# Kernel optimization log

Hardware: AMD Instinct MI355X
Metric: run time of the kernel (lower is better)

Reference implementation:

```python
import jax, jax.numpy as jnp
import numpy as np

K_SIZE = 5
SIGMA_IMG = 0.2
SIGMA_VGG = 0.02
BN_EPS = 1e-5
NORM = 2.0  # 2 * len(GPU_IDS), assuming 1 device


def _window_shifts(x, k):
    # x: (n, C, H, W) -> (n, C, H, W, k*k) neighbor values for every offset in
    # the k x k window, zero-padded at image borders.
    r = k // 2
    n, C, H, W = x.shape
    xp = jnp.pad(x, ((0, 0), (0, 0), (r, r), (r, r)))
    cols = [xp[:, :, di:di + H, dj:dj + W] for di in range(k) for dj in range(k)]
    return jnp.stack(cols, axis=-1)


def _modularity(img, seg, k, sigma):
    # img: (n, C, H, W) feature map; seg: (n, K, H, W) soft assignments.
    n, K, H, W = seg.shape
    seg2 = _window_shifts(seg, k)                                  # (n,K,H,W,kk)
    img2 = _window_shifts(img, k)                                  # (n,C,H,W,kk)
    valid = _window_shifts(jnp.ones((1, 1, H, W), img.dtype), k)[:, 0]  # (1,H,W,kk)
    d2 = ((img[..., None] - img2) ** 2).sum(axis=1)                # (n,H,W,kk)
    w12 = jax.lax.stop_gradient(jnp.exp(-d2 / (2.0 * sigma * sigma)) * valid)
    # numerator: sum over pixels & pairs of p1*p2*w12, per (n, K)
    num = jnp.einsum('nkhw,nkhwp,nhwp->nk', seg, seg2, w12)
    # p1 (sum over pairs of p1/n_pairs) == seg; w1 = sum over pairs of w12
    w1 = w12.sum(axis=-1)                                          # (n,H,W)
    den = jnp.einsum('nhw,nkhw->nk', w1, seg)
    rel = num / den                                                # (n,K)
    return rel.sum(axis=1) / (K * n)                               # (n,)


def _conv(x, w, b):
    y = jax.lax.conv_general_dilated(x, w, (1, 1), 'SAME',
                                     dimension_numbers=('NCHW', 'OIHW', 'NCHW'))
    return y + b[None, :, None, None]


def _maxpool2(x):
    return jax.lax.reduce_window(x, -jnp.inf, jax.lax.max,
                                 (1, 1, 2, 2), (1, 1, 2, 2), 'VALID')


def _avgpool2(x):
    n, c, h, w = x.shape
    return x.reshape(n, c, h // 2, 2, w // 2, 2).mean(axis=(3, 5))


def _vgg8(x, w1, b1, w2, b2, w3, b3, w4, b4):
    # VGG16 features[:8]: conv1_1, conv1_2, maxpool, conv2_1, conv2_2 (relu each)
    x = jax.nn.relu(_conv(x, w1, b1))
    x = jax.nn.relu(_conv(x, w2, b2))
    x = _maxpool2(x)
    x = jax.nn.relu(_conv(x, w3, b3))
    x = jax.nn.relu(_conv(x, w4, b4))
    return x


def _batchnorm(x):
    # fresh BatchNorm2d in training mode (weight=1, bias=0), then detach
    m = x.mean(axis=(0, 2, 3), keepdims=True)
    v = x.var(axis=(0, 2, 3), keepdims=True)
    return jax.lax.stop_gradient((x - m) / jnp.sqrt(v + BN_EPS))


def setup_inputs() -> dict:
    key = jax.random.key(0)
    ks = jax.random.split(key, 6)
    images = jax.random.uniform(ks[0], (4, 3, 128, 128), jnp.float32)
    seg = jax.random.uniform(ks[1], (4, 8, 128, 128), jnp.float32)
    segmentation = seg / seg.sum(axis=1, keepdims=True)
    w1 = jax.random.normal(ks[2], (64, 3, 3, 3), jnp.float32) * 0.1
    w2 = jax.random.normal(ks[3], (64, 64, 3, 3), jnp.float32) * 0.05
    w3 = jax.random.normal(ks[4], (128, 64, 3, 3), jnp.float32) * 0.05
    w4 = jax.random.normal(ks[5], (128, 128, 3, 3), jnp.float32) * 0.03
    return {'images': images, 'segmentation': segmentation,
            'w1': w1, 'b1': jnp.zeros(64), 'w2': w2, 'b2': jnp.zeros(64),
            'w3': w3, 'b3': jnp.zeros(128), 'w4': w4, 'b4': jnp.zeros(128)}


def reference(images, segmentation, w1, b1, w2, b2, w3, b3, w4, b4):
    fich = _batchnorm(_vgg8(images, w1, b1, w2, b2, w3, b3, w4, b4))  # (n,128,64,64)
    images_n = _batchnorm(images)
    down_seg = segmentation
    while down_seg.shape[-1] != fich.shape[-1]:
        down_seg = _avgpool2(down_seg)
    loss = (_modularity(fich, down_seg, K_SIZE, SIGMA_VGG).sum()
            + _modularity(images_n, segmentation, K_SIZE, SIGMA_IMG).sum())
    return loss / NORM
```

## Files before the change

### kernel.cpp

```cpp
#include <hip/hip_runtime.h>
#include <hip/hip_bf16.h>
#include <math.h>

typedef __attribute__((ext_vector_type(8))) short short8;
typedef __attribute__((ext_vector_type(4))) float floatx4;
typedef unsigned short ushortT;

__device__ inline short f2bf(float v) {
    __hip_bfloat16 h = __float2bfloat16(v);
    union { __hip_bfloat16 h; short s; } u; u.h = h; return u.s;
}

#define OFF_C2    0
#define OFF_PAD4  8388608
#define OFF_FICH  12849152
#define OFF_PAD2  21237760
#define OFF_PAD3  29890560
#define OFF_WP2   32120832
#define OFF_WP3   32194560
#define OFF_WP4   32342016
#define OFF_ST    33947648
#define OFF_P64   33951744
#define OFF_P128  33968128
#define OFF_PBN   34033664
#define OFF_PIMG  34295808

__global__ __launch_bounds__(256) void prologue(
    char* ws, const float* __restrict__ images,
    const float* __restrict__ w2, const float* __restrict__ w3,
    const float* __restrict__ w4)
{
    int b = blockIdx.x;
    int tid = threadIdx.x;

    if (b < 162) {
        int t = b * 256 + tid;
        short* base; int Hp, Wp, C; int idx;
        if (t < 16512)      { base = (short*)(ws + OFF_PAD2); Hp = 130; Wp = 130; C = 64;  idx = t; }
        else if (t < 24832) { base = (short*)(ws + OFF_PAD3); Hp = 66;  Wp = 66;  C = 64;  idx = t - 16512; }
        else if (t < 41472) { base = (short*)(ws + OFF_PAD4); Hp = 66;  Wp = 66;  C = 128; idx = t - 24832; }
        else return;
        int c8 = idx % (C / 8); int rest = idx / (C / 8);
        int haloPx = 2 * Wp + 2 * (Hp - 2);
        int p = rest % haloPx; int n = rest / haloPx;
        int y, x;
        if (p < Wp)          { y = 0;      x = p; }
        else if (p < 2 * Wp) { y = Hp - 1; x = p - Wp; }
        else { int j = p - 2 * Wp; y = 1 + (j >> 1); x = (j & 1) ? (Wp - 1) : 0; }
        short8 z = {0, 0, 0, 0, 0, 0, 0, 0};
        *(short8*)&base[((size_t)((n * Hp + y) * Wp) + x) * C + c8 * 8] = z;
        return;
    }
    if (b < 1170) {
        int e = (b - 162) * 256 + tid;
        const float* w; short* wp; int CIN, NTALL;
        if (e < 36864)       { w = w2; wp = (short*)(ws + OFF_WP2); CIN = 64;  NTALL = 4; }
        else if (e < 110592) { e -= 36864;  w = w3; wp = (short*)(ws + OFF_WP3); CIN = 64;  NTALL = 8; }
        else if (e < 258048) { e -= 110592; w = w4; wp = (short*)(ws + OFF_WP4); CIN = 128; NTALL = 8; }
        else return;
        int j = e & 7; int L = (e >> 3) & 63; int rest = e >> 9;
        int nt = rest % NTALL; int rest2 = rest / NTALL;
        int KT = CIN / 32;
        int kt = rest2 % KT; int t = rest2 / KT;
        int oc = nt * 16 + (L & 15);
        int ci = kt * 32 + (L >> 4) * 8 + j;
        wp[e] = f2bf(w[((size_t)oc * CIN + ci) * 9 + t]);
        return;
    }
    {
        float* part = (float*)(ws + OFF_PIMG);
        int bb = b - 1170;
        int c = bb >> 6, chunk = bb & 63;
        int base = chunk * 1024 + tid;
        float s = 0.f, s2 = 0.f;
#pragma unroll
        for (int k = 0; k < 4; ++k) {
            int i = base + k * 256;
            int n = i >> 14, hw = i & 16383;
            float v = images[(((size_t)(n * 3 + c)) << 14) + hw];
            s += v; s2 = fmaf(v, v, s2);
        }
        __shared__ float rs[256], rs2[256];
        rs[tid] = s; rs2[tid] = s2;
        __syncthreads();
        for (int k = 128; k > 0; k >>= 1) {
            if (tid < k) { rs[tid] += rs[tid + k]; rs2[tid] += rs2[tid + k]; }
            __syncthreads();
        }
        if (tid == 0) { part[bb * 2] = rs[0]; part[bb * 2 + 1] = rs2[0]; }
    }
}

__global__ __launch_bounds__(256) void conv1_bf16(
    const float* __restrict__ in, const float* __restrict__ w,
    const float* __restrict__ b, short* __restrict__ outp)
{
    int bid = blockIdx.x;
    int txt = bid & 7; bid >>= 3;
    int tyt = bid & 7; bid >>= 3;
    int ocg = bid & 7; bid >>= 3;
    int n = bid;
    int x0 = txt * 16, y0 = tyt * 16;
    int tid = threadIdx.x;
    int tx = tid & 15, ty = tid >> 4;

    __shared__ float lds[3 * 720];
    for (int i = tid; i < 972; i += 256) {
        int cc = i / 324; int rem = i - cc * 324;
        int r = rem / 18, c = rem - r * 18;
        int y = y0 - 1 + r, x = x0 - 1 + c;
        float v = 0.f;
        if ((unsigned)y < 128u && (unsigned)x < 128u)
            v = in[((size_t)(n * 3 + cc) * 128 + y) * 128 + x];
        lds[cc * 720 + r * 40 + c] = v;
    }
    __syncthreads();

    float acc[8];
#pragma unroll
    for (int oc = 0; oc < 8; ++oc) acc[oc] = 0.f;
    const float* w_g = w + (size_t)(ocg * 8) * 27;
#pragma unroll
    for (int cc = 0; cc < 3; ++cc) {
        const float* base = &lds[cc * 720 + ty * 40 + tx];
        float i00 = base[0],  i01 = base[1],  i02 = base[2];
        float i10 = base[40], i11 = base[41], i12 = base[42];
        float i20 = base[80], i21 = base[81], i22 = base[82];
        const float* wp = w_g + cc * 9;
#pragma unroll
        for (int oc = 0; oc < 8; ++oc) {
            const float* wq = wp + oc * 27;
            float a = acc[oc];
            a = fmaf(wq[0], i00, a); a = fmaf(wq[1], i01, a); a = fmaf(wq[2], i02, a);
            a = fmaf(wq[3], i10, a); a = fmaf(wq[4], i11, a); a = fmaf(wq[5], i12, a);
            a = fmaf(wq[6], i20, a); a = fmaf(wq[7], i21, a); a = fmaf(wq[8], i22, a);
            acc[oc] = a;
        }
    }
    int oy = y0 + ty, ox = x0 + tx;
    short* o = outp + ((size_t)(n * 130 + oy + 1) * 130 + ox + 1) * 64 + ocg * 8;
#pragma unroll
    for (int oc = 0; oc < 8; ++oc) {
        float v = fmaxf(acc[oc] + b[ocg * 8 + oc], 0.f);
        o[oc] = f2bf(v);
    }
}

template<int CIN, int COUT, int H, int W, int OUTMODE>
__global__ __launch_bounds__(256) void conv_mfma2(
    const short* __restrict__ inp, const short* __restrict__ wp,
    const float* __restrict__ bias, void* __restrict__ outv)
{
    constexpr int KT = CIN / 32;
    constexpr int NTALL = COUT / 16;
    constexpr int NTB = COUT / 64;
    constexpr int TPR = W / 64;
    constexpr int Hp = H + 2, Wp = W + 2;

    int bm = blockIdx.x / NTB;
    int bn = blockIdx.x - bm * NTB;
    int n = bm / (H * TPR);
    int rem = bm - n * (H * TPR);
    int y = rem / TPR;
    int x0 = (rem - y * TPR) * 64;

    int tid = threadIdx.x;
    int wv = tid >> 6, lane = tid & 63;
    int lm = lane & 15, q = lane >> 4;
    int px0 = x0 + 16 * wv;
    int ntb = bn * 4;

    floatx4 acc[4];
#pragma unroll
    for (int t = 0; t < 4; ++t) acc[t] = (floatx4){0.f, 0.f, 0.f, 0.f};

    const short* a_m = inp + lm * CIN + q * 8;
    const short* wbase = wp + ((size_t)ntb * 64 + lane) * 8;

    for (int kt = 0; kt < KT; ++kt) {
        int kofs = kt * 32;
#pragma unroll
        for (int r = 0; r < 3; ++r) {
            const short* arow = a_m + (size_t)((n * Hp + y + r) * Wp + px0) * CIN + kofs;
#pragma unroll
            for (int s = 0; s < 3; ++s) {
                short8 av = *(const short8*)(arow + s * CIN);
                const short* bp = wbase + (size_t)(((r * 3 + s) * KT + kt) * NTALL) * 512;
                short8 b0 = *(const short8*)bp;
                short8 b1 = *(const short8*)(bp + 512);
                short8 b2 = *(const short8*)(bp + 1024);
                short8 b3 = *(const short8*)(bp + 1536);
                acc[0] = __builtin_amdgcn_mfma_f32_16x16x32_bf16(av, b0, acc[0], 0, 0, 0);
                acc[1] = __builtin_amdgcn_mfma_f32_16x16x32_bf16(av, b1, acc[1], 0, 0, 0);
                acc[2] = __builtin_amdgcn_mfma_f32_16x16x32_bf16(av, b2, acc[2], 0, 0, 0);
                acc[3] = __builtin_amdgcn_mfma_f32_16x16x32_bf16(av, b3, acc[3], 0, 0, 0);
            }
        }
    }

#pragma unroll
    for (int t = 0; t < 4; ++t) {
        int oc = (ntb + t) * 16 + lm;
        float bs = bias[oc];
#pragma unroll
        for (int i = 0; i < 4; ++i) {
            int px = px0 + q * 4 + i;
            float v = fmaxf(acc[t][i] + bs, 0.f);
            if constexpr (OUTMODE == 0) {
                ((short*)outv)[((size_t)(n * H + y) * W + px) * COUT + oc] = f2bf(v);
            } else if constexpr (OUTMODE == 1) {
                ((short*)outv)[((size_t)(n * Hp + y + 1) * Wp + px + 1) * COUT + oc] = f2bf(v);
            } else {
                ((float*)outv)[((size_t)(n * H + y) * W + px) * COUT + oc] = v;
            }
        }
    }
}

__global__ __launch_bounds__(256) void maxpool_nhwc(const ushortT* __restrict__ in,
                                                    ushortT* __restrict__ outp)
{
    int gid = blockIdx.x * 256 + threadIdx.x;
    int c8 = gid & 7; int rest = gid >> 3;
    int xo = rest & 63, yo = (rest >> 6) & 63, n = rest >> 12;
    const ushortT* p = in + ((size_t)(n * 128 + yo * 2) * 128 + xo * 2) * 64 + c8 * 8;
    const ushortT* p01 = p + 64;
    const ushortT* p10 = p + 128 * 64;
    const ushortT* p11 = p10 + 64;
    ushortT* o = outp + ((size_t)(n * 66 + yo + 1) * 66 + xo + 1) * 64 + c8 * 8;
#pragma unroll
    for (int j = 0; j < 8; ++j) {
        ushortT a = p[j] > p01[j] ? p[j] : p01[j];
        ushortT b = p10[j] > p11[j] ? p10[j] : p11[j];
        o[j] = a > b ? a : b;
    }
}

__global__ __launch_bounds__(256) void bnsum_nhwc(const float* __restrict__ x,
                                                  float* __restrict__ part)
{
    int tid = threadIdx.x;
    int c = tid & 127;
    int h = tid >> 7;
    int p0 = blockIdx.x * 64 + h * 32;
    float s = 0.f, s2 = 0.f;
    for (int p = p0; p < p0 + 32; ++p) {
        float v = x[(size_t)p * 128 + c];
        s += v; s2 = fmaf(v, v, s2);
    }
    __shared__ float rs[256], rs2[256];
    rs[tid] = s; rs2[tid] = s2;
    __syncthreads();
    if (tid < 128) {
        part[(size_t)blockIdx.x * 256 + tid] = rs[tid] + rs[tid + 128];
        part[(size_t)blockIdx.x * 256 + 128 + tid] = rs2[tid] + rs2[tid + 128];
    }
}

__global__ __launch_bounds__(256) void stats_fin(const float* __restrict__ part,
                                                 float* __restrict__ st)
{
    int c = blockIdx.x;
    int t = threadIdx.x;
    float s  = part[(size_t)t * 256 + c];
    float s2 = part[(size_t)t * 256 + 128 + c];
    __shared__ float rs[256], rs2[256];
    rs[t] = s; rs2[t] = s2;
    __syncthreads();
    for (int k = 128; k > 0; k >>= 1) {
        if (t < k) { rs[t] += rs[t + k]; rs2[t] += rs2[t + k]; }
        __syncthreads();
    }
    if (t == 0) {
        float mean = rs[0] * (1.f / 16384.f);
        float var = rs2[0] * (1.f / 16384.f) - mean * mean;
        st[c] = 1.f / sqrtf(var + 1e-5f);
    }
}

__global__ __launch_bounds__(256) void modularity64_v5(
    const float* __restrict__ xt,
    const float* __restrict__ seg,
    const float* __restrict__ st,
    float* __restrict__ part)
{
    __shared__ float fl[4 * 2880];
    __shared__ float sl[8][12][14];

    int tid = threadIdx.x;
    int w = tid >> 6, lane = tid & 63;
    int tx = lane & 7, ty = lane >> 3;
    int obid = blockIdx.x;
    int bid = obid;
    int bx = bid & 7; bid >>= 3;
    int by = bid & 7; bid >>= 3;
    int n = bid;
    int x0 = bx * 8, y0 = by * 8;

    for (int i = tid; i < 8 * 144; i += 256) {
        int k = i / 144;
        int rem = i - k * 144;
        int r = rem / 12, c = rem - r * 12;
        int y = y0 - 2 + r, x = x0 - 2 + c;
        float v = 0.f;
        if ((unsigned)y < 64u && (unsigned)x < 64u) {
            const float* p = seg + ((size_t)(n * 8 + k) * 128 + 2 * y) * 128 + 2 * x;
            float2 a = *(const float2*)p;
            float2 b = *(const float2*)(p + 128);
            v = 0.25f * ((a.x + a.y) + (b.x + b.y));
        }
        sl[k][r][c] = v;
    }

    float* slab = fl + w * 2880;

    float d2p[25];
#pragma unroll
    for (int di = 0; di < 5; ++di)
#pragma unroll
        for (int dj = 0; dj < 5; ++dj) {
            int y2 = y0 + ty + di - 2, x2 = x0 + tx + dj - 2;
            float bias = ((unsigned)y2 < 64u && (unsigned)x2 < 64u) ? 0.f : 1e30f;
            d2p[di * 5 + dj] = (w == 0) ? bias : 0.f;
        }

    for (int r8 = 0; r8 < 2; ++r8) {
        int ch0 = w * 32 + r8 * 16;
        for (int i = lane; i < 576; i += 64) {
            int pix = i >> 2, q = i & 3;
            int r = pix / 12, c = pix - r * 12;
            int y = y0 - 2 + r, x = x0 - 2 + c;
            float4 v = make_float4(0.f, 0.f, 0.f, 0.f);
            if ((unsigned)y < 64u && (unsigned)x < 64u) {
                v = *(const float4*)&xt[((size_t)((n * 64 + y) * 64 + x)) * 128 + ch0 + q * 4];
                float4 sv = *(const float4*)&st[ch0 + q * 4];
                v.x *= sv.x; v.y *= sv.y; v.z *= sv.z; v.w *= sv.w;
            }
            *(float4*)&slab[(r * 12 + c) * 20 + q * 4] = v;
        }

        const float* ctr = &slab[((ty + 2) * 12 + tx + 2) * 20];
        float4 c0 = *(const float4*)(ctr + 0);
        float4 c1 = *(const float4*)(ctr + 4);
        float4 c2 = *(const float4*)(ctr + 8);
        float4 c3 = *(const float4*)(ctr + 12);
#pragma unroll
        for (int di = 0; di < 5; ++di)
#pragma unroll
            for (int dj = 0; dj < 5; ++dj) {
                const float* np = &slab[((ty + di) * 12 + tx + dj) * 20];
                float4 v0 = *(const float4*)(np + 0);
                float4 v1 = *(const float4*)(np + 4);
                float4 v2 = *(const float4*)(np + 8);
                float4 v3 = *(const float4*)(np + 12);
                float d = d2p[di * 5 + dj];
                float e;
                e = c0.x - v0.x; d = fmaf(e, e, d);
                e = c0.y - v0.y; d = fmaf(e, e, d);
                e = c0.z - v0.z; d = fmaf(e, e, d);
                e = c0.w - v0.w; d = fmaf(e, e, d);
                e = c1.x - v1.x; d = fmaf(e, e, d);
                e = c1.y - v1.y; d = fmaf(e, e, d);
                e = c1.z - v1.z; d = fmaf(e, e, d);
                e = c1.w - v1.w; d = fmaf(e, e, d);
                e = c2.x - v2.x; d = fmaf(e, e, d);
                e = c2.y - v2.y; d = fmaf(e, e, d);
                e = c2.z - v2.z; d = fmaf(e, e, d);
                e = c2.w - v2.w; d = fmaf(e, e, d);
                e = c3.x - v3.x; d = fmaf(e, e, d);
                e = c3.y - v3.y; d = fmaf(e, e, d);
                e = c3.z - v3.z; d = fmaf(e, e, d);
                e = c3.w - v3.w; d = fmaf(e, e, d);
                d2p[di * 5 + dj] = d;
            }
    }

#pragma unroll
    for (int j = 0; j < 25; ++j) slab[lane * 25 + j] = d2p[j];
    __syncthreads();

    const float minus_inv2s2 = -1.0f / (2.0f * 0.02f * 0.02f);
    for (int i = tid; i < 1600; i += 256) {
        float d = fl[i] + fl[2880 + i] + fl[5760 + i] + fl[8640 + i];
        fl[i] = expf(d * minus_inv2s2);
    }
    __syncthreads();

    float wgt[25];
    float w1 = 0.f;
#pragma unroll
    for (int j = 0; j < 25; ++j) { wgt[j] = fl[lane * 25 + j]; w1 += wgt[j]; }
#pragma unroll
    for (int kk = 0; kk < 2; ++kk) {
        int k = w * 2 + kk;
        float s = 0.f;
#pragma unroll
        for (int di = 0; di < 5; ++di)
#pragma unroll
            for (int dj = 0; dj < 5; ++dj)
                s = fmaf(wgt[di * 5 + dj], sl[k][ty + di][tx + dj], s);
        float sc = sl[k][ty + 2][tx + 2];
        float numk = s * sc;
        float denk = w1 * sc;
#pragma unroll
        for (int sh = 32; sh > 0; sh >>= 1) {
            numk += __shfl_xor(numk, sh, 64);
            denk += __shfl_xor(denk, sh, 64);
        }
        if (lane == 0) {
            part[(size_t)obid * 16 + k * 2] = numk;
            part[(size_t)obid * 16 + k * 2 + 1] = denk;
        }
    }
}

__global__ __launch_bounds__(256) void modularity128_v6(
    const float* __restrict__ img,
    const float* __restrict__ pimg,
    const float* __restrict__ seg,
    float* __restrict__ part)
{
    __shared__ float il[12][12][4];
    __shared__ float sl[8][12][14];
    __shared__ float stm[6];

    int t = threadIdx.x;
    int w = t >> 6, lane = t & 63;
    int tx = lane & 7, ty = lane >> 3;

    if (t < 64) {
#pragma unroll
        for (int ch = 0; ch < 3; ++ch) {
            float s  = pimg[(ch * 64 + t) * 2];
            float s2 = pimg[(ch * 64 + t) * 2 + 1];
#pragma unroll
            for (int sh = 32; sh > 0; sh >>= 1) {
                s += __shfl_xor(s, sh, 64);
                s2 += __shfl_xor(s2, sh, 64);
            }
            if (t == 0) {
                float mean = s * (1.f / 65536.f);
                float var = s2 * (1.f / 65536.f) - mean * mean;
                stm[ch] = mean;
                stm[3 + ch] = 1.f / sqrtf(var + 1e-5f);
            }
        }
    }

    int obid = blockIdx.x;
    int bid = obid;
    int bx = bid & 15; bid >>= 4;
    int by = bid & 15; bid >>= 4;
    int n = bid;
    int x0 = bx * 8, y0 = by * 8;

    for (int i = t; i < 8 * 144; i += 256) {
        int k = i / 144;
        int rem = i - k * 144;
        int r = rem / 12, c = rem - r * 12;
        int y = y0 - 2 + r, x = x0 - 2 + c;
        float v = 0.f;
        if ((unsigned)y < 128u && (unsigned)x < 128u)
            v = seg[((size_t)(n * 8 + k) * 128 + y) * 128 + x];
        sl[k][r][c] = v;
    }
    __syncthreads();

    float mn0 = stm[0], mn1 = stm[1], mn2 = stm[2];
    float rs0 = stm[3], rs1 = stm[4], rs2 = stm[5];

    for (int i = t; i < 432; i += 256) {
        int ch = i / 144; int pix = i - ch * 144;
        int r = pix / 12, c = pix - r * 12;
        int y = y0 - 2 + r, x = x0 - 2 + c;
        float v = 0.f;
        if ((unsigned)y < 128u && (unsigned)x < 128u) {
            float raw = img[(((size_t)(n * 3 + ch)) << 14) + y * 128 + x];
            float mn = ch == 0 ? mn0 : (ch == 1 ? mn1 : mn2);
            float rs = ch == 0 ? rs0 : (ch == 1 ? rs1 : rs2);
            v = (raw - mn) * rs;
        }
        il[r][c][ch] = v;
    }
    __syncthreads();

    const float minus_inv2s2 = -1.0f / (2.0f * 0.2f * 0.2f);
    float c0 = il[ty + 2][tx + 2][0];
    float c1 = il[ty + 2][tx + 2][1];
    float c2 = il[ty + 2][tx + 2][2];

    float wgt[25];
    float w1 = 0.f;
#pragma unroll
    for (int di = 0; di < 5; ++di)
#pragma unroll
        for (int dj = 0; dj < 5; ++dj) {
            int y2 = y0 + ty + di - 2, x2 = x0 + tx + dj - 2;
            float bias = ((unsigned)y2 < 128u && (unsigned)x2 < 128u) ? 0.f : 1e30f;
            const float* np = &il[ty + di][tx + dj][0];
            float e0 = c0 - np[0], e1 = c1 - np[1], e2 = c2 - np[2];
            float d = bias + fmaf(e2, e2, fmaf(e1, e1, e0 * e0));
            float wv = expf(d * minus_inv2s2);
            wgt[di * 5 + dj] = wv;
            w1 += wv;
        }

#pragma unroll
    for (int kk = 0; kk < 2; ++kk) {
        int k = w * 2 + kk;
        float s = 0.f;
#pragma unroll
        for (int di = 0; di < 5; ++di)
#pragma unroll
            for (int dj = 0; dj < 5; ++dj)
                s = fmaf(wgt[di * 5 + dj], sl[k][ty + di][tx + dj], s);
        float sc = sl[k][ty + 2][tx + 2];
        float numk = s * sc;
        float denk = w1 * sc;
#pragma unroll
        for (int sft = 32; sft > 0; sft >>= 1) {
            numk += __shfl_xor(numk, sft, 64);
            denk += __shfl_xor(denk, sft, 64);
        }
        if (lane == 0) {
            part[(size_t)obid * 16 + k * 2] = numk;
            part[(size_t)obid * 16 + k * 2 + 1] = denk;
        }
    }
}

__global__ __launch_bounds__(1024) void reduce_finalize(
    const float* __restrict__ p64, const float* __restrict__ p128,
    float* __restrict__ out)
{
    int t = threadIdx.x;
    int j = t >> 4, s = t & 15;
    float num = 0.f, den = 0.f;
    if (j < 32) {
        int n = j >> 3, k = j & 7;
#pragma unroll
        for (int i = 0; i < 4; ++i) {
            int b = s * 4 + i;
            const float* p = p64 + ((size_t)(n * 64 + b)) * 16 + k * 2;
            num += p[0]; den += p[1];
        }
    } else {
        int jj = j - 32; int n = jj >> 3, k = jj & 7;
#pragma unroll
        for (int i = 0; i < 16; ++i) {
            int b = s * 16 + i;
            const float* p = p128 + ((size_t)(n * 256 + b)) * 16 + k * 2;
            num += p[0]; den += p[1];
        }
    }
#pragma unroll
    for (int sh = 8; sh > 0; sh >>= 1) {
        num += __shfl_xor(num, sh, 16);
        den += __shfl_xor(den, sh, 16);
    }
    __shared__ float rn[64], rd[64];
    if (s == 0) { rn[j] = num; rd[j] = den; }
    __syncthreads();
    if (t < 64) {
        float v = rn[t] / rd[t];
#pragma unroll
        for (int sh = 32; sh > 0; sh >>= 1) v += __shfl_xor(v, sh, 64);
        if (t == 0) out[0] = v * (1.0f / 64.0f);
    }
}

extern "C" void kernel_launch(void* const* d_in, const int* in_sizes, int n_in,
                              void* d_out, int out_size, void* d_ws, size_t ws_size,
                              hipStream_t stream)
{
    const float* images = (const float*)d_in[0];
    const float* seg    = (const float*)d_in[1];
    const float* w1 = (const float*)d_in[2]; const float* b1 = (const float*)d_in[3];
    const float* w2 = (const float*)d_in[4]; const float* b2 = (const float*)d_in[5];
    const float* w3 = (const float*)d_in[6]; const float* b3 = (const float*)d_in[7];
    const float* w4 = (const float*)d_in[8]; const float* b4 = (const float*)d_in[9];
    float* out = (float*)d_out;
    char* ws = (char*)d_ws;
    short* C2   = (short*)(ws + OFF_C2);
    short* PAD2 = (short*)(ws + OFF_PAD2);
    short* PAD3 = (short*)(ws + OFF_PAD3);
    short* PAD4 = (short*)(ws + OFF_PAD4);
    float* FICH = (float*)(ws + OFF_FICH);
    short* WP2  = (short*)(ws + OFF_WP2);
    short* WP3  = (short*)(ws + OFF_WP3);
    short* WP4  = (short*)(ws + OFF_WP4);
    float* ST   = (float*)(ws + OFF_ST);
    float* P64  = (float*)(ws + OFF_P64);
    float* P128 = (float*)(ws + OFF_P128);
    float* PBN  = (float*)(ws + OFF_PBN);
    float* PIMG = (float*)(ws + OFF_PIMG);

    prologue<<<1362, 256, 0, stream>>>(ws, images, w2, w3, w4);

    conv1_bf16<<<2048, 256, 0, stream>>>(images, w1, b1, PAD2);
    conv_mfma2<64, 64, 128, 128, 0><<<1024, 256, 0, stream>>>(PAD2, WP2, b2, C2);
    maxpool_nhwc<<<512, 256, 0, stream>>>((const ushortT*)C2, (ushortT*)PAD3);
    conv_mfma2<64, 128, 64, 64, 1><<<512, 256, 0, stream>>>(PAD3, WP3, b3, PAD4);
    conv_mfma2<128, 128, 64, 64, 2><<<512, 256, 0, stream>>>(PAD4, WP4, b4, FICH);

    bnsum_nhwc<<<256, 256, 0, stream>>>(FICH, PBN);
    stats_fin<<<128, 256, 0, stream>>>(PBN, ST);

    modularity64_v5<<<256, 256, 0, stream>>>(FICH, seg, ST, P64);
    modularity128_v6<<<1024, 256, 0, stream>>>(images, PIMG, seg, P128);
    reduce_finalize<<<1, 1024, 0, stream>>>(P64, P128, out);
}
```

Baseline: 185.5 us.

## Fuse conv1 into prologue, maxpool into conv2, BN stats into conv4, merge modularity

Conv1 now runs as extra blocks of the prologue kernel. Conv2 is rewritten to compute two output rows per block and apply the 2x2 maxpool in registers, writing straight into the padded conv3 input, so the full-resolution intermediate buffer disappears. Conv4 accumulates per-channel sum and sum-of-squares for batchnorm in its epilogue, removing the separate pass that re-read the feature map. The two modularity kernels are merged into one interleaved launch. Together these cut launch count and global memory round trips, at the cost of more complex kernels, a new partial-sum layout for the stats, and some loss of tiling flexibility in conv2.

Result: faster. 166.7 us (-10.1%).

```diff
diff --git a/kernel.cpp b/kernel.cpp
--- a/kernel.cpp
+++ b/kernel.cpp
@@ -27,11 +27,67 @@
 
 __global__ __launch_bounds__(256) void prologue(
     char* ws, const float* __restrict__ images,
+    const float* __restrict__ w1, const float* __restrict__ b1,
     const float* __restrict__ w2, const float* __restrict__ w3,
     const float* __restrict__ w4)
 {
+    __shared__ float plds[3 * 720];
+    __shared__ float rs[256], rs2[256];
+
     int b = blockIdx.x;
     int tid = threadIdx.x;
+
+    if (b >= 1362) {
+        int bid = b - 1362;
+        int txt = bid & 7; bid >>= 3;
+        int tyt = bid & 7; bid >>= 3;
+        int ocg = bid & 7; bid >>= 3;
+        int n = bid;
+        int x0 = txt * 16, y0 = tyt * 16;
+        int tx = tid & 15, ty = tid >> 4;
+        short* outp = (short*)(ws + OFF_PAD2);
+
+        for (int i = tid; i < 972; i += 256) {
+            int cc = i / 324; int rem = i - cc * 324;
+            int r = rem / 18, c = rem - r * 18;
+            int y = y0 - 1 + r, x = x0 - 1 + c;
+            float v = 0.f;
+            if ((unsigned)y < 128u && (unsigned)x < 128u)
+                v = images[((size_t)(n * 3 + cc) * 128 + y) * 128 + x];
+            plds[cc * 720 + r * 40 + c] = v;
+        }
+        __syncthreads();
+
+        float acc[8];
+#pragma unroll
+        for (int oc = 0; oc < 8; ++oc) acc[oc] = 0.f;
+        const float* w_g = w1 + (size_t)(ocg * 8) * 27;
+#pragma unroll
+        for (int cc = 0; cc < 3; ++cc) {
+            const float* base = &plds[cc * 720 + ty * 40 + tx];
+            float i00 = base[0],  i01 = base[1],  i02 = base[2];
+            float i10 = base[40], i11 = base[41], i12 = base[42];
+            float i20 = base[80], i21 = base[81], i22 = base[82];
+            const float* wp = w_g + cc * 9;
+#pragma unroll
+            for (int oc = 0; oc < 8; ++oc) {
+                const float* wq = wp + oc * 27;
+                float a = acc[oc];
+                a = fmaf(wq[0], i00, a); a = fmaf(wq[1], i01, a); a = fmaf(wq[2], i02, a);
+                a = fmaf(wq[3], i10, a); a = fmaf(wq[4], i11, a); a = fmaf(wq[5], i12, a);
+                a = fmaf(wq[6], i20, a); a = fmaf(wq[7], i21, a); a = fmaf(wq[8], i22, a);
+                acc[oc] = a;
+            }
+        }
+        int oy = y0 + ty, ox = x0 + tx;
+        short* o = outp + ((size_t)(n * 130 + oy + 1) * 130 + ox + 1) * 64 + ocg * 8;
+#pragma unroll
+        for (int oc = 0; oc < 8; ++oc) {
+            float v = fmaxf(acc[oc] + b1[ocg * 8 + oc], 0.f);
+            o[oc] = f2bf(v);
+        }
+        return;
+    }
 
     if (b < 162) {
         int t = b * 256 + tid;
@@ -80,7 +136,6 @@
             float v = images[(((size_t)(n * 3 + c)) << 14) + hw];
             s += v; s2 = fmaf(v, v, s2);
         }
-        __shared__ float rs[256], rs2[256];
         rs[tid] = s; rs2[tid] = s2;
         __syncthreads();
         for (int k = 128; k > 0; k >>= 1) {
@@ -91,58 +146,85 @@
     }
 }
 
-__global__ __launch_bounds__(256) void conv1_bf16(
-    const float* __restrict__ in, const float* __restrict__ w,
-    const float* __restrict__ b, short* __restrict__ outp)
-{
+__global__ __launch_bounds__(256) void conv2_pool(
+    const short* __restrict__ inp,
+    const short* __restrict__ wp,
+    const float* __restrict__ bias,
+    short* __restrict__ outp)
+{
+    constexpr int CIN = 64;
+    constexpr int Hp = 130, Wp = 130;
+
     int bid = blockIdx.x;
-    int txt = bid & 7; bid >>= 3;
-    int tyt = bid & 7; bid >>= 3;
-    int ocg = bid & 7; bid >>= 3;
+    int xtb = bid & 1; bid >>= 1;
+    int yp = bid & 63; bid >>= 6;
     int n = bid;
-    int x0 = txt * 16, y0 = tyt * 16;
+    int y0 = yp * 2;
+    int x0 = xtb * 64;
+
     int tid = threadIdx.x;
-    int tx = tid & 15, ty = tid >> 4;
-
-    __shared__ float lds[3 * 720];
-    for (int i = tid; i < 972; i += 256) {
-        int cc = i / 324; int rem = i - cc * 324;
-        int r = rem / 18, c = rem - r * 18;
-        int y = y0 - 1 + r, x = x0 - 1 + c;
-        float v = 0.f;
-        if ((unsigned)y < 128u && (unsigned)x < 128u)
-            v = in[((size_t)(n * 3 + cc) * 128 + y) * 128 + x];
-        lds[cc * 720 + r * 40 + c] = v;
-    }
-    __syncthreads();
-
-    float acc[8];
-#pragma unroll
-    for (int oc = 0; oc < 8; ++oc) acc[oc] = 0.f;
-    const float* w_g = w + (size_t)(ocg * 8) * 27;
-#pragma unroll
-    for (int cc = 0; cc < 3; ++cc) {
-        const float* base = &lds[cc * 720 + ty * 40 + tx];
-        float i00 = base[0],  i01 = base[1],  i02 = base[2];
-        float i10 = base[40], i11 = base[41], i12 = base[42];
-        float i20 = base[80], i21 = base[81], i22 = base[82];
-        const float* wp = w_g + cc * 9;
-#pragma unroll
-        for (int oc = 0; oc < 8; ++oc) {
-            const float* wq = wp + oc * 27;
-            float a = acc[oc];
-            a = fmaf(wq[0], i00, a); a = fmaf(wq[1], i01, a); a = fmaf(wq[2], i02, a);
-            a = fmaf(wq[3], i10, a); a = fmaf(wq[4], i11, a); a = fmaf(wq[5], i12, a);
-            a = fmaf(wq[6], i20, a); a = fmaf(wq[7], i21, a); a = fmaf(wq[8], i22, a);
-            acc[oc] = a;
-        }
-    }
-    int oy = y0 + ty, ox = x0 + tx;
-    short* o = outp + ((size_t)(n * 130 + oy + 1) * 130 + ox + 1) * 64 + ocg * 8;
-#pragma unroll
-    for (int oc = 0; oc < 8; ++oc) {
-        float v = fmaxf(acc[oc] + b[ocg * 8 + oc], 0.f);
-        o[oc] = f2bf(v);
+    int wv = tid >> 6, lane = tid & 63;
+    int lm = lane & 15, q = lane >> 4;
+    int px0 = x0 + 16 * wv;
+
+    floatx4 acc0[4], acc1[4];
+#pragma unroll
+    for (int t = 0; t < 4; ++t) {
+        acc0[t] = (floatx4){0.f, 0.f, 0.f, 0.f};
+        acc1[t] = (floatx4){0.f, 0.f, 0.f, 0.f};
+    }
+
+    const short* a_m = inp + lm * CIN + q * 8;
+    const short* wbase = wp + (size_t)lane * 8;
+
+    for (int kt = 0; kt < 2; ++kt) {
+        int kofs = kt * 32;
+#pragma unroll
+        for (int s = 0; s < 3; ++s) {
+            const short* acol = a_m + ((size_t)((n * Hp + y0) * Wp) + px0 + s) * CIN + kofs;
+            short8 av0 = *(const short8*)(acol);
+            short8 av1 = *(const short8*)(acol + (size_t)Wp * CIN);
+            short8 av2 = *(const short8*)(acol + (size_t)2 * Wp * CIN);
+            short8 av3 = *(const short8*)(acol + (size_t)3 * Wp * CIN);
+#pragma unroll
+            for (int r = 0; r < 3; ++r) {
+                const short* bp = wbase + (size_t)(((r * 3 + s) * 2 + kt) * 4) * 512;
+                short8 b0 = *(const short8*)bp;
+                short8 b1 = *(const short8*)(bp + 512);
+                short8 b2 = *(const short8*)(bp + 1024);
+                short8 b3 = *(const short8*)(bp + 1536);
+                short8 ar  = (r == 0) ? av0 : ((r == 1) ? av1 : av2);
+                short8 ar1 = (r == 0) ? av1 : ((r == 1) ? av2 : av3);
+                acc0[0] = __builtin_amdgcn_mfma_f32_16x16x32_bf16(ar, b0, acc0[0], 0, 0, 0);
+                acc0[1] = __builtin_amdgcn_mfma_f32_16x16x32_bf16(ar, b1, acc0[1], 0, 0, 0);
+                acc0[2] = __builtin_amdgcn_mfma_f32_16x16x32_bf16(ar, b2, acc0[2], 0, 0, 0);
+                acc0[3] = __builtin_amdgcn_mfma_f32_16x16x32_bf16(ar, b3, acc0[3], 0, 0, 0);
+                acc1[0] = __builtin_amdgcn_mfma_f32_16x16x32_bf16(ar1, b0, acc1[0], 0, 0, 0);
+                acc1[1] = __builtin_amdgcn_mfma_f32_16x16x32_bf16(ar1, b1, acc1[1], 0, 0, 0);
+                acc1[2] = __builtin_amdgcn_mfma_f32_16x16x32_bf16(ar1, b2, acc1[2], 0, 0, 0);
+                acc1[3] = __builtin_amdgcn_mfma_f32_16x16x32_bf16(ar1, b3, acc1[3], 0, 0, 0);
+            }
+        }
+    }
+
+    int ox = (px0 + q * 4) >> 1;
+#pragma unroll
+    for (int t = 0; t < 4; ++t) {
+        int oc = t * 16 + lm;
+        float bs = bias[oc];
+        float v00 = fmaxf(acc0[t][0] + bs, 0.f);
+        float v01 = fmaxf(acc0[t][1] + bs, 0.f);
+        float v02 = fmaxf(acc0[t][2] + bs, 0.f);
+        float v03 = fmaxf(acc0[t][3] + bs, 0.f);
+        float v10 = fmaxf(acc1[t][0] + bs, 0.f);
+        float v11 = fmaxf(acc1[t][1] + bs, 0.f);
+        float v12 = fmaxf(acc1[t][2] + bs, 0.f);
+        float v13 = fmaxf(acc1[t][3] + bs, 0.f);
+        float m0 = fmaxf(fmaxf(v00, v01), fmaxf(v10, v11));
+        float m1 = fmaxf(fmaxf(v02, v03), fmaxf(v12, v13));
+        short* o = outp + ((size_t)(n * 66 + yp + 1) * 66 + ox + 1) * 64 + oc;
+        o[0]  = f2bf(m0);
+        o[64] = f2bf(m1);
     }
 }
 
@@ -217,43 +299,79 @@
     }
 }
 
-__global__ __launch_bounds__(256) void maxpool_nhwc(const ushortT* __restrict__ in,
-                                                    ushortT* __restrict__ outp)
-{
-    int gid = blockIdx.x * 256 + threadIdx.x;
-    int c8 = gid & 7; int rest = gid >> 3;
-    int xo = rest & 63, yo = (rest >> 6) & 63, n = rest >> 12;
-    const ushortT* p = in + ((size_t)(n * 128 + yo * 2) * 128 + xo * 2) * 64 + c8 * 8;
-    const ushortT* p01 = p + 64;
-    const ushortT* p10 = p + 128 * 64;
-    const ushortT* p11 = p10 + 64;
-    ushortT* o = outp + ((size_t)(n * 66 + yo + 1) * 66 + xo + 1) * 64 + c8 * 8;
-#pragma unroll
-    for (int j = 0; j < 8; ++j) {
-        ushortT a = p[j] > p01[j] ? p[j] : p01[j];
-        ushortT b = p10[j] > p11[j] ? p10[j] : p11[j];
-        o[j] = a > b ? a : b;
-    }
-}
-
-__global__ __launch_bounds__(256) void bnsum_nhwc(const float* __restrict__ x,
-                                                  float* __restrict__ part)
-{
+__global__ __launch_bounds__(256) void conv4_bn(
+    const short* __restrict__ inp,
+    const short* __restrict__ wp,
+    const float* __restrict__ bias,
+    float* __restrict__ out,
+    float* __restrict__ part)
+{
+    constexpr int CIN = 128;
+    constexpr int Hp = 66, Wp = 66;
+
+    int bm = blockIdx.x >> 1;
+    int bn = blockIdx.x & 1;
+    int n = bm >> 6;
+    int y = bm & 63;
+
     int tid = threadIdx.x;
-    int c = tid & 127;
-    int h = tid >> 7;
-    int p0 = blockIdx.x * 64 + h * 32;
-    float s = 0.f, s2 = 0.f;
-    for (int p = p0; p < p0 + 32; ++p) {
-        float v = x[(size_t)p * 128 + c];
-        s += v; s2 = fmaf(v, v, s2);
-    }
-    __shared__ float rs[256], rs2[256];
-    rs[tid] = s; rs2[tid] = s2;
+    int wv = tid >> 6, lane = tid & 63;
+    int lm = lane & 15, q = lane >> 4;
+    int px0 = 16 * wv;
+    int ntb = bn * 4;
+
+    floatx4 acc[4];
+#pragma unroll
+    for (int t = 0; t < 4; ++t) acc[t] = (floatx4){0.f, 0.f, 0.f, 0.f};
+
+    const short* a_m = inp + lm * CIN + q * 8;
+    const short* wbase = wp + ((size_t)ntb * 64 + lane) * 8;
+
+    for (int kt = 0; kt < 4; ++kt) {
+        int kofs = kt * 32;
+#pragma unroll
+        for (int r = 0; r < 3; ++r) {
+            const short* arow = a_m + (size_t)((n * Hp + y + r) * Wp + px0) * CIN + kofs;
+#pragma unroll
+            for (int s = 0; s < 3; ++s) {
+                short8 av = *(const short8*)(arow + s * CIN);
+                const short* bp = wbase + (size_t)(((r * 3 + s) * 4 + kt) * 8) * 512;
+                short8 b0 = *(const short8*)bp;
+                short8 b1 = *(const short8*)(bp + 512);
+                short8 b2 = *(const short8*)(bp + 1024);
+                short8 b3 = *(const short8*)(bp + 1536);
+                acc[0] = __builtin_amdgcn_mfma_f32_16x16x32_bf16(av, b0, acc[0], 0, 0, 0);
+                acc[1] = __builtin_amdgcn_mfma_f32_16x16x32_bf16(av, b1, acc[1], 0, 0, 0);
+                acc[2] = __builtin_amdgcn_mfma_f32_16x16x32_bf16(av, b2, acc[2], 0, 0, 0);
+                acc[3] = __builtin_amdgcn_mfma_f32_16x16x32_bf16(av, b3, acc[3], 0, 0, 0);
+            }
+        }
+    }
+
+    __shared__ float ps[4][4][16], ps2[4][4][16];
+#pragma unroll
+    for (int t = 0; t < 4; ++t) {
+        int oc = (ntb + t) * 16 + lm;
+        float bs = bias[oc];
+        float sv = 0.f, sv2 = 0.f;
+#pragma unroll
+        for (int i = 0; i < 4; ++i) {
+            int px = px0 + q * 4 + i;
+            float v = fmaxf(acc[t][i] + bs, 0.f);
+            out[((size_t)(n * 64 + y) * 64 + px) * 128 + oc] = v;
+            sv += v; sv2 = fmaf(v, v, sv2);
+        }
+        sv  += __shfl_xor(sv, 16, 64);  sv  += __shfl_xor(sv, 32, 64);
+        sv2 += __shfl_xor(sv2, 16, 64); sv2 += __shfl_xor(sv2, 32, 64);
+        if (q == 0) { ps[wv][t][lm] = sv; ps2[wv][t][lm] = sv2; }
+    }
     __syncthreads();
-    if (tid < 128) {
-        part[(size_t)blockIdx.x * 256 + tid] = rs[tid] + rs[tid + 128];
-        part[(size_t)blockIdx.x * 256 + 128 + tid] = rs2[tid] + rs2[tid + 128];
+    if (tid < 64) {
+        int t_ = tid >> 4, lm_ = tid & 15;
+        float a  = ps[0][t_][lm_] + ps[1][t_][lm_] + ps[2][t_][lm_] + ps[3][t_][lm_];
+        float a2 = ps2[0][t_][lm_] + ps2[1][t_][lm_] + ps2[2][t_][lm_] + ps2[3][t_][lm_];
+        part[(size_t)blockIdx.x * 128 + tid * 2]     = a;
+        part[(size_t)blockIdx.x * 128 + tid * 2 + 1] = a2;
     }
 }
 
@@ -262,8 +380,9 @@
 {
     int c = blockIdx.x;
     int t = threadIdx.x;
-    float s  = part[(size_t)t * 256 + c];
-    float s2 = part[(size_t)t * 256 + 128 + c];
+    int bn = c >> 6, cl = c & 63;
+    float s  = part[(size_t)(t * 2 + bn) * 128 + cl * 2];
+    float s2 = part[(size_t)(t * 2 + bn) * 128 + cl * 2 + 1];
     __shared__ float rs[256], rs2[256];
     rs[t] = s; rs2[t] = s2;
     __syncthreads();
@@ -278,19 +397,15 @@
     }
 }
 
-__global__ __launch_bounds__(256) void modularity64_v5(
-    const float* __restrict__ xt,
-    const float* __restrict__ seg,
-    const float* __restrict__ st,
-    float* __restrict__ part)
-{
-    __shared__ float fl[4 * 2880];
-    __shared__ float sl[8][12][14];
-
+__device__ __forceinline__ void mod64_body(
+    int obid,
+    const float* __restrict__ xt, const float* __restrict__ seg,
+    const float* __restrict__ st, float* __restrict__ part,
+    float* fl, float (*sl)[12][14])
+{
     int tid = threadIdx.x;
     int w = tid >> 6, lane = tid & 63;
     int tx = lane & 7, ty = lane >> 3;
-    int obid = blockIdx.x;
     int bid = obid;
     int bx = bid & 7; bid >>= 3;
     int by = bid & 7; bid >>= 3;
@@ -414,16 +529,12 @@
     }
 }
 
-__global__ __launch_bounds__(256) void modularity128_v6(
-    const float* __restrict__ img,
-    const float* __restrict__ pimg,
-    const float* __restrict__ seg,
-    float* __restrict__ part)
-{
-    __shared__ float il[12][12][4];
-    __shared__ float sl[8][12][14];
-    __shared__ float stm[6];
-
+__device__ __forceinline__ void mod128_body(
+    int obid,
+    const float* __restrict__ img, const float* __restrict__ pimg,
+    const float* __restrict__ seg, float* __restrict__ part,
+    float (*il)[12][4], float (*sl)[12][14], float* stm)
+{
     int t = threadIdx.x;
     int w = t >> 6, lane = t & 63;
     int tx = lane & 7, ty = lane >> 3;
@@ -447,7 +558,6 @@
         }
     }
 
-    int obid = blockIdx.x;
     int bid = obid;
     int bx = bid & 15; bid >>= 4;
     int by = bid & 15; bid >>= 4;
@@ -529,6 +639,29 @@
     }
 }
 
+__global__ __launch_bounds__(256) void modularity_all(
+    const float* __restrict__ xt,
+    const float* __restrict__ seg,
+    const float* __restrict__ st,
+    const float* __restrict__ img,
+    const float* __restrict__ pimg,
+    float* __restrict__ p64, float* __restrict__ p128)
+{
+    __shared__ float fl[4 * 2880];
+    __shared__ float sl[8][12][14];
+    __shared__ float stm[6];
+
+    int bid = blockIdx.x;
+    int g = bid / 5;
+    int r5 = bid - g * 5;
+    if (r5 == 0) {
+        mod64_body(g, xt, seg, st, p64, fl, sl);
+    } else {
+        mod128_body(bid - g - 1, img, pimg, seg, p128,
+                    (float(*)[12][4])fl, sl, stm);
+    }
+}
+
 __global__ __launch_bounds__(1024) void reduce_finalize(
     const float* __restrict__ p64, const float* __restrict__ p128,
     float* __restrict__ out)
@@ -581,7 +714,6 @@
     const float* w4 = (const float*)d_in[8]; const float* b4 = (const float*)d_in[9];
     float* out = (float*)d_out;
     char* ws = (char*)d_ws;
-    short* C2   = (short*)(ws + OFF_C2);
     short* PAD2 = (short*)(ws + OFF_PAD2);
     short* PAD3 = (short*)(ws + OFF_PAD3);
     short* PAD4 = (short*)(ws + OFF_PAD4);
@@ -595,18 +727,11 @@
     float* PBN  = (float*)(ws + OFF_PBN);
     float* PIMG = (float*)(ws + OFF_PIMG);
 
-    prologue<<<1362, 256, 0, stream>>>(ws, images, w2, w3, w4);
-
-    conv1_bf16<<<2048, 256, 0, stream>>>(images, w1, b1, PAD2);
-    conv_mfma2<64, 64, 128, 128, 0><<<1024, 256, 0, stream>>>(PAD2, WP2, b2, C2);
-    maxpool_nhwc<<<512, 256, 0, stream>>>((const ushortT*)C2, (ushortT*)PAD3);
+    prologue<<<3410, 256, 0, stream>>>(ws, images, w1, b1, w2, w3, w4);
+    conv2_pool<<<512, 256, 0, stream>>>(PAD2, WP2, b2, PAD3);
     conv_mfma2<64, 128, 64, 64, 1><<<512, 256, 0, stream>>>(PAD3, WP3, b3, PAD4);
-    conv_mfma2<128, 128, 64, 64, 2><<<512, 256, 0, stream>>>(PAD4, WP4, b4, FICH);
-
-    bnsum_nhwc<<<256, 256, 0, stream>>>(FICH, PBN);
+    conv4_bn<<<512, 256, 0, stream>>>(PAD4, WP4, b4, FICH, PBN);
     stats_fin<<<128, 256, 0, stream>>>(PBN, ST);
-
-    modularity64_v5<<<256, 256, 0, stream>>>(FICH, seg, ST, P64);
-    modularity128_v6<<<1024, 256, 0, stream>>>(images, PIMG, seg, P128);
+    modularity_all<<<1280, 256, 0, stream>>>(FICH, seg, ST, images, PIMG, P64, P128);
     reduce_finalize<<<1, 1024, 0, stream>>>(P64, P128, out);
 }
```
